# Kernel optimization log

Hardware: AMD Instinct MI355X
Metric: run time of the kernel (lower is better)

Reference implementation:

```python
import jax, jax.numpy as jnp
import numpy as np

B, S, D, K = 8, 2048, 512, 64

def setup_inputs() -> dict:
    key = jax.random.key(0)
    k1, k2, k3 = jax.random.split(key, 3)
    # glorot_uniform for weights, zeros for biases (matching Keras build)
    lim = float(np.sqrt(6.0 / (D + K)))
    return {
        "inputs": jax.random.normal(k1, (B, S, D), dtype=jnp.float32),
        "key_extract": jax.random.uniform(k2, (D, K), dtype=jnp.float32, minval=-lim, maxval=lim),
        "key_bias": jnp.zeros((1, K), dtype=jnp.float32),
        "query_extract": jax.random.uniform(k3, (D, K), dtype=jnp.float32, minval=-lim, maxval=lim),
        "query_bias": jnp.zeros((1, K), dtype=jnp.float32),
    }

def reference(inputs, key_extract, key_bias, query_extract, query_bias):
    # keys/query: [B, S, K]
    keys = jnp.einsum("bsd,dk->bsk", inputs, key_extract) + key_bias
    query = jnp.einsum("bsd,dk->bsk", inputs, query_extract) + query_bias
    # logits: [B, S, S] = query @ keys^T (no 1/sqrt(K) scaling in original)
    logits = jnp.einsum("bqk,bsk->bqs", query, keys)
    # NON-STANDARD: softmax over axis=1 (the query axis), not the last axis
    attn = jax.nn.softmax(logits, axis=1)
    # weighted_input: [B, S, D], raw inputs used as V
    return jnp.einsum("bqs,bsd->bqd", attn, inputs)
```

## Files before the change

### kernel.cpp

```cpp
#include <hip/hip_runtime.h>
#include <hip/hip_bf16.h>

#define Bn 8
#define Sn 2048
#define Dn 512
#define Kn 64

typedef _Float16 half8 __attribute__((ext_vector_type(8)));
typedef _Float16 half4v __attribute__((ext_vector_type(4)));
typedef __fp16 fp16x2 __attribute__((ext_vector_type(2)));
typedef float f32x4 __attribute__((ext_vector_type(4)));

#define MFMA16(a,b,c) __builtin_amdgcn_mfma_f32_16x16x32_f16(a,b,c,0,0,0)
#define LOG2E 1.4426950408889634f
#define EXP2(x) __builtin_amdgcn_exp2f(x)

__device__ __forceinline__ half8 ldfrag(const _Float16* base, int row, int k8){
    const int scol = k8 ^ (row & 7);
    return *(const half8*)((const char*)base + row*128 + scol*16);
}


__global__ __launch_bounds__(256) void wtrans_kernel(
    const float* __restrict__ Wk, const float* __restrict__ Wq,
    _Float16* __restrict__ Wt16)
{
    const int n = blockIdx.x;
    const int t = threadIdx.x;
    const float* src = (n < 64) ? Wq : Wk;
    const int nn = n & 63;
    #pragma unroll
    for (int i = 0; i < 2; ++i){
        const int k = t + 256*i;
        Wt16[(size_t)n*Dn + k] = (_Float16)src[(size_t)k*Kn + nn];
    }
}

__global__ __launch_bounds__(256, 2) void prep_kernel(
    const float* __restrict__ X, const _Float16* __restrict__ Wt16,
    const float* __restrict__ bk, const float* __restrict__ bq,
    _Float16* __restrict__ Qh2, _Float16* __restrict__ Kh2,
    _Float16* __restrict__ Vt2)
{
    __shared__ _Float16 Xt[2][32*64];
    const int bid = blockIdx.x;
    const int b = bid & 7, sb32 = bid >> 3;
    const int tid = threadIdx.x, lane = tid & 63, w = tid >> 6;
    const int l15 = lane & 15, l4 = lane >> 4;

    const int srow = tid >> 3, sg = tid & 7;
    const float* Xs = X + ((size_t)(b*Sn + sb32*32) + srow)*Dn + sg*8;
    const int sdst = srow*128 + (((sg ^ (srow & 7) ^ (srow >> 3)) & 7) * 16);

    const int n0 = w*32 + l15;
    const _Float16* Wp0 = Wt16 + (size_t)n0*Dn + l4*8;
    const _Float16* Wp1 = Wp0 + (size_t)16*Dn;

    f32x4 acc[2][2];
    #pragma unroll
    for (int i = 0; i < 2; ++i)
        #pragma unroll
        for (int j = 0; j < 2; ++j){ f32x4 z = {0.f,0.f,0.f,0.f}; acc[i][j] = z; }

    {
        const float4 v0 = *(const float4*)(Xs);
        const float4 v1 = *(const float4*)(Xs + 4);
        half8 h;
        h[0]=(_Float16)v0.x; h[1]=(_Float16)v0.y; h[2]=(_Float16)v0.z; h[3]=(_Float16)v0.w;
        h[4]=(_Float16)v1.x; h[5]=(_Float16)v1.y; h[6]=(_Float16)v1.z; h[7]=(_Float16)v1.w;
        *(half8*)((char*)Xt[0] + sdst) = h;
    }
    __syncthreads();

    const int dcol = w*16 + l15;
    #pragma unroll
    for (int kc = 0; kc < 8; ++kc){
        const _Float16* XtC = Xt[kc & 1];
        float4 nv0, nv1;
        if (kc < 7){
            nv0 = *(const float4*)(Xs + (kc+1)*64);
            nv1 = *(const float4*)(Xs + (kc+1)*64 + 4);
        }
        const half8 wf00 = *(const half8*)(Wp0 + kc*64);
        const half8 wf01 = *(const half8*)(Wp0 + kc*64 + 32);
        const half8 wf10 = *(const half8*)(Wp1 + kc*64);
        const half8 wf11 = *(const half8*)(Wp1 + kc*64 + 32);
        #pragma unroll
        for (int ks = 0; ks < 2; ++ks){
            #pragma unroll
            for (int qt = 0; qt < 2; ++qt){
                const int rw = qt*16 + l15;
                const int g = ((ks*4 + l4) ^ (rw & 7) ^ (rw >> 3)) & 7;
                const half8 a = *(const half8*)((const char*)XtC + rw*128 + g*16);
                acc[qt][0] = MFMA16(a, ks ? wf01 : wf00, acc[qt][0]);
                acc[qt][1] = MFMA16(a, ks ? wf11 : wf10, acc[qt][1]);
            }
        }
        {
            half8 hv;
            #pragma unroll
            for (int e = 0; e < 8; ++e){
                const int rw = l4*8 + e;
                const int g = ((dcol >> 3) ^ e ^ l4) & 7;
                hv[e] = XtC[rw*64 + g*8 + (dcol & 7)];
            }
            const size_t G = (((size_t)(b*32 + (sb32 >> 1))*2 + (sb32 & 1))*32 + kc*4 + w)*64 + lane;
            *(half8*)(Vt2 + G*8) = hv;
        }
        if (kc < 7){
            half8 h;
            h[0]=(_Float16)nv0.x; h[1]=(_Float16)nv0.y; h[2]=(_Float16)nv0.z; h[3]=(_Float16)nv0.w;
            h[4]=(_Float16)nv1.x; h[5]=(_Float16)nv1.y; h[6]=(_Float16)nv1.z; h[7]=(_Float16)nv1.w;
            *(half8*)((char*)Xt[(kc+1) & 1] + sdst) = h;
        }
        __syncthreads();
    }

    _Float16* tile16 = &Xt[0][0];
    #pragma unroll
    for (int qt = 0; qt < 2; ++qt){
        const int ql = qt*16 + l4*4;
        #pragma unroll
        for (int nt = 0; nt < 2; ++nt){
            const int n = w*32 + nt*16 + l15;
            const bool isQ = (n < 64);
            const float bias = isQ ? bq[n] : bk[n - 64];
            const float scale = isQ ? LOG2E : 1.0f;
            #pragma unroll
            for (int r = 0; r < 4; ++r)
                tile16[(ql + r)*128 + n] = (_Float16)((acc[qt][nt][r] + bias) * scale);
        }
    }
    __syncthreads();
    #pragma unroll
    for (int i = 0; i < 2; ++i){
        const int g = tid + 256*i;
        const int isK = g >> 8, qtl = (g >> 7) & 1, ks = (g >> 6) & 1, ln = g & 63;
        const int l4g = ln >> 4, l15g = ln & 15;
        const half8 h = *(const half8*)&tile16[(qtl*16 + l15g)*128 + isK*64 + ks*32 + l4g*8];
        const size_t tg = (size_t)b*128 + sb32*2 + qtl;
        _Float16* dst = (isK ? Kh2 : Qh2) + ((tg*2 + ks)*64 + ln)*8;
        *(half8*)dst = h;
    }
}

#define SBODY(QC0,QC1,QC2,QC3, QN0,QN1,QN2,QN3) do { \
    QN0 = *(const half8*)(Qp); \
    QN1 = *(const half8*)(Qp + 1024); \
    QN2 = *(const half8*)(Qp + 2048); \
    QN3 = *(const half8*)(Qp + 3072); \
    Qp += 8192; \
    f32x4 c0 = cinit, c1 = cinit; \
    c0 = MFMA16(ka0, QC0, c0); c0 = MFMA16(ka1, QC1, c0); \
    c1 = MFMA16(ka0, QC2, c1); c1 = MFMA16(ka1, QC3, c1); \
    _Pragma("unroll") \
    for (int r = 0; r < 4; ++r) \
        z[r] += EXP2(c0[r]) + EXP2(c1[r]); \
} while(0)

__global__ __launch_bounds__(512, 2) void stats_kernel(
    const _Float16* __restrict__ Qh2, const _Float16* __restrict__ Kh2,
    float* __restrict__ CS)
{
    __shared__ float zred[2][64];
    const int bid = blockIdx.x;
    const int b = bid & 7, stb = bid >> 3;
    const int tid = threadIdx.x, lane = tid & 63, w = tid >> 6;
    const int l15 = lane & 15, l4 = lane >> 4;
    const int sw = w & 3, qh = w >> 2, qh2 = qh*2;

    const half8 ka0 = *(const half8*)(Kh2 + ((size_t)((b*128 + stb*4 + sw)*2 + 0)*64 + lane)*8);
    const half8 ka1 = *(const half8*)(Kh2 + ((size_t)((b*128 + stb*4 + sw)*2 + 1)*64 + lane)*8);

    const char* Qp = (const char*)Qh2 + (size_t)(b*128 + qh2)*2048 + lane*16;

    const f32x4 cinit = {-64.f, -64.f, -64.f, -64.f};
    float z[4] = {0.f, 0.f, 0.f, 0.f};

    half8 qbA0, qbA1, qbA2, qbA3, qbB0, qbB1, qbB2, qbB3;
    qbA0 = *(const half8*)(Qp);
    qbA1 = *(const half8*)(Qp + 1024);
    qbA2 = *(const half8*)(Qp + 2048);
    qbA3 = *(const half8*)(Qp + 3072);
    Qp += 8192;

    for (int qc = 0; qc < 32; qc += 2){
        SBODY(qbA0,qbA1,qbA2,qbA3, qbB0,qbB1,qbB2,qbB3);
        SBODY(qbB0,qbB1,qbB2,qbB3, qbA0,qbA1,qbA2,qbA3);
    }
    #pragma unroll
    for (int d = 1; d < 16; d <<= 1)
        #pragma unroll
        for (int r = 0; r < 4; ++r)
            z[r] += __shfl_xor(z[r], d);
    if (l15 == 0){
        const int sl = sw*16 + l4*4;
        #pragma unroll
        for (int r = 0; r < 4; ++r) zred[qh][sl+r] = z[r];
    }
    __syncthreads();
    if (tid < 64)
        CS[b*Sn + stb*64 + tid] = -(64.0f + __log2f(zred[0][tid] + zred[1][tid]));
}

#define WRP(PT, QT, C) do { \
    const float e0 = EXP2(C[0]); \
    const float e1 = EXP2(C[1]); \
    const float e2 = EXP2(C[2]); \
    const float e3 = EXP2(C[3]); \
    const fp16x2 plo = __builtin_amdgcn_cvt_pkrtz(e0, e1); \
    const fp16x2 phi = __builtin_amdgcn_cvt_pkrtz(e2, e3); \
    uint2 pu; \
    pu.x = __builtin_bit_cast(unsigned int, plo); \
    pu.y = __builtin_bit_cast(unsigned int, phi); \
    *(uint2*)((char*)(PT) + (QT)*2048 + pw_base) = pu; \
} while(0)

#define ABODY(KA, KAN, VB, VBN, CSA, CSN, PT) do { \
    f32x4 c0 = {CSA.x, CSA.y, CSA.z, CSA.w}; \
    f32x4 c1 = c0, c2 = c0, c3 = c0; \
    c0 = MFMA16(KA[0], qb[0][0], c0); c0 = MFMA16(KA[1], qb[0][1], c0); \
    c1 = MFMA16(KA[0], qb[1][0], c1); c1 = MFMA16(KA[1], qb[1][1], c1); \
    c2 = MFMA16(KA[0], qb[2][0], c2); c2 = MFMA16(KA[1], qb[2][1], c2); \
    c3 = MFMA16(KA[0], qb[3][0], c3); c3 = MFMA16(KA[1], qb[3][1], c3); \
    KAN[0] = *(const half8*)(Kp); \
    KAN[1] = *(const half8*)(Kp + 1024); \
    Kp += 8192; \
    CSN = *(const float4*)Cp; Cp += 64; \
    WRP(PT, 0, c0); WRP(PT, 1, c1); \
    WRP(PT, 2, c2); WRP(PT, 3, c3); \
    asm volatile("s_waitcnt lgkmcnt(0)\n\ts_barrier" ::: "memory"); \
    _Pragma("unroll") \
    for (int d_ = 0; d_ < 4; ++d_){ \
        VBN[d_]   = *(const half8*)(Vp0 + d_*1024); \
        VBN[4+d_] = *(const half8*)(Vp1 + d_*1024); \
    } \
    Vp0 += 65536; Vp1 += 65536; \
    __builtin_amdgcn_s_setprio(1); \
    { const char* PB = (const char*)(PT); \
      _Pragma("unroll") \
      for (int ks = 0; ks < 2; ++ks){ \
        const int po = ks ? paoff1 : paoff0; \
        const half8 pa0 = *(const half8*)(PB + 0*2048 + po); \
        const half8 pa1 = *(const half8*)(PB + 1*2048 + po); \
        const half8 pa2 = *(const half8*)(PB + 2*2048 + po); \
        const half8 pa3 = *(const half8*)(PB + 3*2048 + po); \
        _Pragma("unroll") \
        for (int d_ = 0; d_ < 4; ++d_){ \
            acc[0][d_] = MFMA16(pa0, VB[ks*4+d_], acc[0][d_]); \
            acc[1][d_] = MFMA16(pa1, VB[ks*4+d_], acc[1][d_]); \
            acc[2][d_] = MFMA16(pa2, VB[ks*4+d_], acc[2][d_]); \
            acc[3][d_] = MFMA16(pa3, VB[ks*4+d_], acc[3][d_]); \
        } \
      } } \
    __builtin_amdgcn_s_setprio(0); \
} while(0)

__global__ __launch_bounds__(256, 2) void attn_kernel(
    const _Float16* __restrict__ Qh2, const _Float16* __restrict__ Kh2,
    const _Float16* __restrict__ Vt2, const float* __restrict__ CS,
    float* __restrict__ out)
{
    __shared__ _Float16 Pt[2][64*64];
    const int bid = blockIdx.x;
    const int b  = bid & 7;
    const int qi = (bid >> 3) & 31;
    const int dh = bid >> 8;
    const int q0 = qi * 64;
    const int tid = threadIdx.x, lane = tid & 63, w = tid >> 6;
    const int l15 = lane & 15, l4 = lane >> 4;
    const int soff = w*16 + l4*4;
    const int sb2  = soff * 2;
    const int pw_base = l15*128 + (sb2 ^ ((l15 & 7) << 4));
    const int paoff0  = l15*128 + ((l4 ^ (l15 & 7)) << 4);
    const int paoff1  = paoff0 ^ 64;

    const size_t qgb = (size_t)b*128 + qi*4;
    half8 qb[4][2];
    #pragma unroll
    for (int qt = 0; qt < 4; ++qt)
        #pragma unroll
        for (int ks = 0; ks < 2; ++ks)
            qb[qt][ks] = *(const half8*)(Qh2 + (((qgb + qt)*2 + ks)*64 + lane)*8);

    const char* Kp  = (const char*)Kh2 + (size_t)(b*128 + w)*2048 + lane*16;
    const char* Vp0 = (const char*)Vt2 + (size_t)(b*2048 + dh*16 + w*4)*1024 + lane*16;
    const char* Vp1 = Vp0 + 32768;
    const float* Cp = CS + b*Sn + soff;

    half8 kaA[2], kaB[2], vbA[8], vbB[8];
    float4 csA, csB;
    kaA[0] = *(const half8*)(Kp);
    kaA[1] = *(const half8*)(Kp + 1024);
    Kp += 8192;
    #pragma unroll
    for (int d_ = 0; d_ < 4; ++d_){
        vbA[d_]   = *(const half8*)(Vp0 + d_*1024);
        vbA[4+d_] = *(const half8*)(Vp1 + d_*1024);
    }
    Vp0 += 65536; Vp1 += 65536;
    csA = *(const float4*)Cp; Cp += 64;

    f32x4 acc[4][4];
    #pragma unroll
    for (int i = 0; i < 4; ++i)
        #pragma unroll
        for (int j = 0; j < 4; ++j){ f32x4 zz4 = {0.f,0.f,0.f,0.f}; acc[i][j] = zz4; }

    for (int it = 0; it < 16; ++it){
        ABODY(kaA, kaB, vbA, vbB, csA, csB, Pt[0]);
        ABODY(kaB, kaA, vbB, vbA, csB, csA, Pt[1]);
    }

    float* ob = out + (size_t)(b*Sn + q0)*Dn + dh*256 + w*64;
    #pragma unroll
    for (int qt = 0; qt < 4; ++qt){
        const int q = qt*16 + l4*4;
        #pragma unroll
        for (int d_ = 0; d_ < 4; ++d_){
            #pragma unroll
            for (int r = 0; r < 4; ++r)
                ob[(size_t)(q + r)*Dn + d_*16 + l15] = acc[qt][d_][r];
        }
    }
}

extern "C" void kernel_launch(void* const* d_in, const int* in_sizes, int n_in,
                              void* d_out, int out_size, void* d_ws, size_t ws_size,
                              hipStream_t stream)
{
    const float* X  = (const float*)d_in[0];
    const float* Wk = (const float*)d_in[1];
    const float* bk = (const float*)d_in[2];
    const float* Wq = (const float*)d_in[3];
    const float* bq = (const float*)d_in[4];
    float* out = (float*)d_out;

    char* ws = (char*)d_ws;
    _Float16* Qh2  = (_Float16*)ws;
    _Float16* Kh2  = (_Float16*)(ws + ((size_t)2 << 20));
    _Float16* Vt2  = (_Float16*)(ws + ((size_t)4 << 20));
    float*    CS   = (float*)(ws + ((size_t)20 << 20));
    _Float16* Wt16 = (_Float16*)(ws + ((size_t)20 << 20) + (2 << 16));

    wtrans_kernel<<<dim3(128), dim3(256), 0, stream>>>(Wk, Wq, Wt16);
    prep_kernel<<<dim3(Bn*(Sn/32)), dim3(256), 0, stream>>>(X, Wt16, bk, bq, Qh2, Kh2, Vt2);
    stats_kernel<<<dim3(Bn*(Sn/64)), dim3(512), 0, stream>>>(Qh2, Kh2, CS);
    attn_kernel<<<dim3(Bn*(Sn/64)*2), dim3(256), 0, stream>>>(Qh2, Kh2, Vt2, CS, out);
}
```

Measured before the change: 73.73 us.

## Process two 64-key tiles per barrier step in attention kernel

Doubles the key-tile width handled per loop step from 64 to 128 keys. P is written to a larger 64x128 shared tile with a new swizzle, so only one barrier is needed per 128 keys instead of per 64. The V loads are split into a mid-step load and a next-step prefetch. This halves the barrier count and gives more MFMA work between syncs, at the cost of more registers (extra K fragments and V buffers) and twice the LDS, which may reduce occupancy below 2 blocks per CU.

```diff
diff --git a/kernel.cpp b/kernel.cpp
--- a/kernel.cpp
+++ b/kernel.cpp
@@ -203,7 +203,7 @@
         CS[b*Sn + stb*64 + tid] = -(64.0f + __log2f(zred[0][tid] + zred[1][tid]));
 }
 
-#define WRP(PT, QT, C) do { \
+#define WRP(PT, QT, C, PWO) do { \
     const float e0 = EXP2(C[0]); \
     const float e1 = EXP2(C[1]); \
     const float e2 = EXP2(C[2]); \
@@ -213,44 +213,83 @@
     uint2 pu; \
     pu.x = __builtin_bit_cast(unsigned int, plo); \
     pu.y = __builtin_bit_cast(unsigned int, phi); \
-    *(uint2*)((char*)(PT) + (QT)*2048 + pw_base) = pu; \
+    *(uint2*)((char*)(PT) + (QT)*4096 + (PWO)) = pu; \
 } while(0)
 
-#define ABODY(KA, KAN, VB, VBN, CSA, CSN, PT) do { \
-    f32x4 c0 = {CSA.x, CSA.y, CSA.z, CSA.w}; \
+#define SSTEP(PT, KA, KAN, CSA0, CSA1, CSN0, CSN1, VC, VN) do { \
+    __builtin_amdgcn_s_setprio(1); \
+    f32x4 c0 = {CSA0.x, CSA0.y, CSA0.z, CSA0.w}; \
     f32x4 c1 = c0, c2 = c0, c3 = c0; \
     c0 = MFMA16(KA[0], qb[0][0], c0); c0 = MFMA16(KA[1], qb[0][1], c0); \
     c1 = MFMA16(KA[0], qb[1][0], c1); c1 = MFMA16(KA[1], qb[1][1], c1); \
     c2 = MFMA16(KA[0], qb[2][0], c2); c2 = MFMA16(KA[1], qb[2][1], c2); \
     c3 = MFMA16(KA[0], qb[3][0], c3); c3 = MFMA16(KA[1], qb[3][1], c3); \
+    f32x4 d0 = {CSA1.x, CSA1.y, CSA1.z, CSA1.w}; \
+    f32x4 d1 = d0, d2 = d0, d3 = d0; \
+    d0 = MFMA16(KA[2], qb[0][0], d0); d0 = MFMA16(KA[3], qb[0][1], d0); \
+    d1 = MFMA16(KA[2], qb[1][0], d1); d1 = MFMA16(KA[3], qb[1][1], d1); \
+    d2 = MFMA16(KA[2], qb[2][0], d2); d2 = MFMA16(KA[3], qb[2][1], d2); \
+    d3 = MFMA16(KA[2], qb[3][0], d3); d3 = MFMA16(KA[3], qb[3][1], d3); \
+    __builtin_amdgcn_s_setprio(0); \
     KAN[0] = *(const half8*)(Kp); \
     KAN[1] = *(const half8*)(Kp + 1024); \
-    Kp += 8192; \
-    CSN = *(const float4*)Cp; Cp += 64; \
-    WRP(PT, 0, c0); WRP(PT, 1, c1); \
-    WRP(PT, 2, c2); WRP(PT, 3, c3); \
+    KAN[2] = *(const half8*)(Kp + 8192); \
+    KAN[3] = *(const half8*)(Kp + 8192 + 1024); \
+    Kp += 16384; \
+    CSN0 = *(const float4*)Cp; \
+    CSN1 = *(const float4*)(Cp + 64); \
+    Cp += 128; \
+    WRP(PT, 0, c0, pw0); WRP(PT, 1, c1, pw0); \
+    WRP(PT, 2, c2, pw0); WRP(PT, 3, c3, pw0); \
+    WRP(PT, 0, d0, pw1); WRP(PT, 1, d1, pw1); \
+    WRP(PT, 2, d2, pw1); WRP(PT, 3, d3, pw1); \
     asm volatile("s_waitcnt lgkmcnt(0)\n\ts_barrier" ::: "memory"); \
+    half8 vm[8]; \
     _Pragma("unroll") \
     for (int d_ = 0; d_ < 4; ++d_){ \
-        VBN[d_]   = *(const half8*)(Vp0 + d_*1024); \
-        VBN[4+d_] = *(const half8*)(Vp1 + d_*1024); \
+        vm[d_]   = *(const half8*)(Vp0 + d_*1024); \
+        vm[4+d_] = *(const half8*)(Vp1 + d_*1024); \
     } \
     Vp0 += 65536; Vp1 += 65536; \
     __builtin_amdgcn_s_setprio(1); \
     { const char* PB = (const char*)(PT); \
       _Pragma("unroll") \
       for (int ks = 0; ks < 2; ++ks){ \
-        const int po = ks ? paoff1 : paoff0; \
-        const half8 pa0 = *(const half8*)(PB + 0*2048 + po); \
-        const half8 pa1 = *(const half8*)(PB + 1*2048 + po); \
-        const half8 pa2 = *(const half8*)(PB + 2*2048 + po); \
-        const half8 pa3 = *(const half8*)(PB + 3*2048 + po); \
+        const int po = pa[ks]; \
+        const half8 pa0 = *(const half8*)(PB + 0*4096 + po); \
+        const half8 pa1 = *(const half8*)(PB + 1*4096 + po); \
+        const half8 pa2 = *(const half8*)(PB + 2*4096 + po); \
+        const half8 pa3 = *(const half8*)(PB + 3*4096 + po); \
         _Pragma("unroll") \
         for (int d_ = 0; d_ < 4; ++d_){ \
-            acc[0][d_] = MFMA16(pa0, VB[ks*4+d_], acc[0][d_]); \
-            acc[1][d_] = MFMA16(pa1, VB[ks*4+d_], acc[1][d_]); \
-            acc[2][d_] = MFMA16(pa2, VB[ks*4+d_], acc[2][d_]); \
-            acc[3][d_] = MFMA16(pa3, VB[ks*4+d_], acc[3][d_]); \
+            acc[0][d_] = MFMA16(pa0, VC[ks*4+d_], acc[0][d_]); \
+            acc[1][d_] = MFMA16(pa1, VC[ks*4+d_], acc[1][d_]); \
+            acc[2][d_] = MFMA16(pa2, VC[ks*4+d_], acc[2][d_]); \
+            acc[3][d_] = MFMA16(pa3, VC[ks*4+d_], acc[3][d_]); \
+        } \
+      } } \
+    __builtin_amdgcn_s_setprio(0); \
+    _Pragma("unroll") \
+    for (int d_ = 0; d_ < 4; ++d_){ \
+        VN[d_]   = *(const half8*)(Vp0 + d_*1024); \
+        VN[4+d_] = *(const half8*)(Vp1 + d_*1024); \
+    } \
+    Vp0 += 65536; Vp1 += 65536; \
+    __builtin_amdgcn_s_setprio(1); \
+    { const char* PB = (const char*)(PT); \
+      _Pragma("unroll") \
+      for (int ks = 0; ks < 2; ++ks){ \
+        const int po = pa[2+ks]; \
+        const half8 pa0 = *(const half8*)(PB + 0*4096 + po); \
+        const half8 pa1 = *(const half8*)(PB + 1*4096 + po); \
+        const half8 pa2 = *(const half8*)(PB + 2*4096 + po); \
+        const half8 pa3 = *(const half8*)(PB + 3*4096 + po); \
+        _Pragma("unroll") \
+        for (int d_ = 0; d_ < 4; ++d_){ \
+            acc[0][d_] = MFMA16(pa0, vm[ks*4+d_], acc[0][d_]); \
+            acc[1][d_] = MFMA16(pa1, vm[ks*4+d_], acc[1][d_]); \
+            acc[2][d_] = MFMA16(pa2, vm[ks*4+d_], acc[2][d_]); \
+            acc[3][d_] = MFMA16(pa3, vm[ks*4+d_], acc[3][d_]); \
         } \
       } } \
     __builtin_amdgcn_s_setprio(0); \
@@ -261,7 +300,7 @@
     const _Float16* __restrict__ Vt2, const float* __restrict__ CS,
     float* __restrict__ out)
 {
-    __shared__ _Float16 Pt[2][64*64];
+    __shared__ _Float16 Pt[2][64*128];
     const int bid = blockIdx.x;
     const int b  = bid & 7;
     const int qi = (bid >> 3) & 31;
@@ -270,10 +309,13 @@
     const int tid = threadIdx.x, lane = tid & 63, w = tid >> 6;
     const int l15 = lane & 15, l4 = lane >> 4;
     const int soff = w*16 + l4*4;
-    const int sb2  = soff * 2;
-    const int pw_base = l15*128 + (sb2 ^ ((l15 & 7) << 4));
-    const int paoff0  = l15*128 + ((l4 ^ (l15 & 7)) << 4);
-    const int paoff1  = paoff0 ^ 64;
+
+    const int pw0 = l15*256 + (((w*2 + (l4 >> 1)) ^ (l15 & 7)) << 4) + ((l4 & 1) << 3);
+    const int pw1 = pw0 + 128;
+    int pa[4];
+    #pragma unroll
+    for (int j = 0; j < 4; ++j)
+        pa[j] = l15*256 + (((j >> 1)*8 + (((j & 1)*4 + l4) ^ (l15 & 7))) << 4);
 
     const size_t qgb = (size_t)b*128 + qi*4;
     half8 qb[4][2];
@@ -288,18 +330,22 @@
     const char* Vp1 = Vp0 + 32768;
     const float* Cp = CS + b*Sn + soff;
 
-    half8 kaA[2], kaB[2], vbA[8], vbB[8];
-    float4 csA, csB;
+    half8 kaA[4], kaB[4], vbA[8], vbB[8];
+    float4 csA0, csA1, csB0, csB1;
     kaA[0] = *(const half8*)(Kp);
     kaA[1] = *(const half8*)(Kp + 1024);
-    Kp += 8192;
+    kaA[2] = *(const half8*)(Kp + 8192);
+    kaA[3] = *(const half8*)(Kp + 8192 + 1024);
+    Kp += 16384;
+    csA0 = *(const float4*)Cp;
+    csA1 = *(const float4*)(Cp + 64);
+    Cp += 128;
     #pragma unroll
     for (int d_ = 0; d_ < 4; ++d_){
         vbA[d_]   = *(const half8*)(Vp0 + d_*1024);
         vbA[4+d_] = *(const half8*)(Vp1 + d_*1024);
     }
     Vp0 += 65536; Vp1 += 65536;
-    csA = *(const float4*)Cp; Cp += 64;
 
     f32x4 acc[4][4];
     #pragma unroll
@@ -307,9 +353,9 @@
         #pragma unroll
         for (int j = 0; j < 4; ++j){ f32x4 zz4 = {0.f,0.f,0.f,0.f}; acc[i][j] = zz4; }
 
-    for (int it = 0; it < 16; ++it){
-        ABODY(kaA, kaB, vbA, vbB, csA, csB, Pt[0]);
-        ABODY(kaB, kaA, vbB, vbA, csB, csA, Pt[1]);
+    for (int it = 0; it < 8; ++it){
+        SSTEP(Pt[0], kaA, kaB, csA0, csA1, csB0, csB1, vbA, vbB);
+        SSTEP(Pt[1], kaB, kaA, csB0, csB1, csA0, csA1, vbB, vbA);
     }
 
     float* ob = out + (size_t)(b*Sn + q0)*Dn + dh*256 + w*64;
```

Measured after the change: 74.70 us. No clear change (+1.3%).

## Split stats kernel over query chunks with LDS-staged Q and partial-sum finalize

Applied to the files above, without the earlier changes.

The column-softmax stats pass now has each block load a 256-query chunk of Q into LDS with direct global-to-LDS loads. Each wave keeps four key tiles in registers and reuses every Q fragment across them, instead of streaming the full Q from global memory per key tile. Partial exp sums per query chunk go to a workspace buffer, and a new small kernel adds them and takes the log. This cuts redundant Q traffic and raises register reuse per MFMA, at the cost of an extra kernel launch, more register pressure and a workspace round trip.

```diff
diff --git a/kernel.cpp b/kernel.cpp
--- a/kernel.cpp
+++ b/kernel.cpp
@@ -14,6 +14,12 @@
 #define MFMA16(a,b,c) __builtin_amdgcn_mfma_f32_16x16x32_f16(a,b,c,0,0,0)
 #define LOG2E 1.4426950408889634f
 #define EXP2(x) __builtin_amdgcn_exp2f(x)
+
+__device__ __forceinline__ void glds16(const void* g, void* l){
+    __builtin_amdgcn_global_load_lds(
+        (const __attribute__((address_space(1))) unsigned int*)g,
+        (__attribute__((address_space(3))) unsigned int*)l, 16, 0, 0);
+}
 
 __device__ __forceinline__ half8 ldfrag(const _Float16* base, int row, int k8){
     const int scol = k8 ^ (row & 7);
@@ -144,63 +150,78 @@
     }
 }
 
-#define SBODY(QC0,QC1,QC2,QC3, QN0,QN1,QN2,QN3) do { \
-    QN0 = *(const half8*)(Qp); \
-    QN1 = *(const half8*)(Qp + 1024); \
-    QN2 = *(const half8*)(Qp + 2048); \
-    QN3 = *(const half8*)(Qp + 3072); \
-    Qp += 8192; \
-    f32x4 c0 = cinit, c1 = cinit; \
-    c0 = MFMA16(ka0, QC0, c0); c0 = MFMA16(ka1, QC1, c0); \
-    c1 = MFMA16(ka0, QC2, c1); c1 = MFMA16(ka1, QC3, c1); \
-    _Pragma("unroll") \
-    for (int r = 0; r < 4; ++r) \
-        z[r] += EXP2(c0[r]) + EXP2(c1[r]); \
-} while(0)
-
-__global__ __launch_bounds__(512, 2) void stats_kernel(
+__global__ __launch_bounds__(512) void stats_kernel(
     const _Float16* __restrict__ Qh2, const _Float16* __restrict__ Kh2,
-    float* __restrict__ CS)
-{
-    __shared__ float zred[2][64];
+    float* __restrict__ Zp)
+{
+    __shared__ _Float16 Qs[256*64];
     const int bid = blockIdx.x;
-    const int b = bid & 7, stb = bid >> 3;
+    const int b = bid & 7, ss = (bid >> 3) & 3, qc = bid >> 5;
     const int tid = threadIdx.x, lane = tid & 63, w = tid >> 6;
     const int l15 = lane & 15, l4 = lane >> 4;
-    const int sw = w & 3, qh = w >> 2, qh2 = qh*2;
-
-    const half8 ka0 = *(const half8*)(Kh2 + ((size_t)((b*128 + stb*4 + sw)*2 + 0)*64 + lane)*8);
-    const half8 ka1 = *(const half8*)(Kh2 + ((size_t)((b*128 + stb*4 + sw)*2 + 1)*64 + lane)*8);
-
-    const char* Qp = (const char*)Qh2 + (size_t)(b*128 + qh2)*2048 + lane*16;
+
+    const char* Qsrc = (const char*)Qh2 + (size_t)(b*128 + qc*16)*2048;
+    #pragma unroll
+    for (int i = 0; i < 4; ++i)
+        glds16(Qsrc + tid*16 + i*8192, (char*)Qs + w*1024 + i*8192);
+
+    half8 ka[4][2];
+    const char* Kb = (const char*)Kh2 + (size_t)(b*128 + ss*32 + w*4)*2048 + lane*16;
+    #pragma unroll
+    for (int st = 0; st < 4; ++st)
+        #pragma unroll
+        for (int ks = 0; ks < 2; ++ks)
+            ka[st][ks] = *(const half8*)(Kb + st*2048 + ks*1024);
+
+    __syncthreads();
 
     const f32x4 cinit = {-64.f, -64.f, -64.f, -64.f};
-    float z[4] = {0.f, 0.f, 0.f, 0.f};
-
-    half8 qbA0, qbA1, qbA2, qbA3, qbB0, qbB1, qbB2, qbB3;
-    qbA0 = *(const half8*)(Qp);
-    qbA1 = *(const half8*)(Qp + 1024);
-    qbA2 = *(const half8*)(Qp + 2048);
-    qbA3 = *(const half8*)(Qp + 3072);
-    Qp += 8192;
-
-    for (int qc = 0; qc < 32; qc += 2){
-        SBODY(qbA0,qbA1,qbA2,qbA3, qbB0,qbB1,qbB2,qbB3);
-        SBODY(qbB0,qbB1,qbB2,qbB3, qbA0,qbA1,qbA2,qbA3);
+    float z[4][4];
+    #pragma unroll
+    for (int st = 0; st < 4; ++st)
+        #pragma unroll
+        for (int r = 0; r < 4; ++r) z[st][r] = 0.f;
+
+    const char* Qb = (const char*)Qs + lane*16;
+    for (int qt = 0; qt < 16; ++qt){
+        const half8 qb0 = *(const half8*)(Qb + qt*2048);
+        const half8 qb1 = *(const half8*)(Qb + qt*2048 + 1024);
+        #pragma unroll
+        for (int st = 0; st < 4; ++st){
+            f32x4 c = cinit;
+            c = MFMA16(ka[st][0], qb0, c);
+            c = MFMA16(ka[st][1], qb1, c);
+            #pragma unroll
+            for (int r = 0; r < 4; ++r)
+                z[st][r] += EXP2(c[r]);
+        }
     }
     #pragma unroll
     for (int d = 1; d < 16; d <<= 1)
         #pragma unroll
-        for (int r = 0; r < 4; ++r)
-            z[r] += __shfl_xor(z[r], d);
+        for (int st = 0; st < 4; ++st)
+            #pragma unroll
+            for (int r = 0; r < 4; ++r)
+                z[st][r] += __shfl_xor(z[st][r], d);
     if (l15 == 0){
-        const int sl = sw*16 + l4*4;
-        #pragma unroll
-        for (int r = 0; r < 4; ++r) zred[qh][sl+r] = z[r];
-    }
-    __syncthreads();
-    if (tid < 64)
-        CS[b*Sn + stb*64 + tid] = -(64.0f + __log2f(zred[0][tid] + zred[1][tid]));
+        float* zp = Zp + (((size_t)(qc*8 + b)) << 11) + ss*512 + w*64 + l4*4;
+        #pragma unroll
+        for (int st = 0; st < 4; ++st)
+            #pragma unroll
+            for (int r = 0; r < 4; ++r)
+                zp[st*16 + r] = z[st][r];
+    }
+}
+
+__global__ __launch_bounds__(256) void csfin_kernel(
+    const float* __restrict__ Zp, float* __restrict__ CS)
+{
+    const int idx = blockIdx.x*256 + threadIdx.x;
+    float zsum = 0.f;
+    #pragma unroll
+    for (int qc = 0; qc < 8; ++qc)
+        zsum += Zp[(qc << 14) + idx];
+    CS[idx] = -(64.0f + __log2f(zsum));
 }
 
 #define WRP(PT, QT, C) do { \
@@ -342,9 +363,11 @@
     _Float16* Vt2  = (_Float16*)(ws + ((size_t)4 << 20));
     float*    CS   = (float*)(ws + ((size_t)20 << 20));
     _Float16* Wt16 = (_Float16*)(ws + ((size_t)20 << 20) + (2 << 16));
+    float*    Zp   = (float*)(ws + ((size_t)21 << 20));
 
     wtrans_kernel<<<dim3(128), dim3(256), 0, stream>>>(Wk, Wq, Wt16);
     prep_kernel<<<dim3(Bn*(Sn/32)), dim3(256), 0, stream>>>(X, Wt16, bk, bq, Qh2, Kh2, Vt2);
-    stats_kernel<<<dim3(Bn*(Sn/64)), dim3(512), 0, stream>>>(Qh2, Kh2, CS);
+    stats_kernel<<<dim3(256), dim3(512), 0, stream>>>(Qh2, Kh2, Zp);
+    csfin_kernel<<<dim3(64), dim3(256), 0, stream>>>(Zp, CS);
     attn_kernel<<<dim3(Bn*(Sn/64)*2), dim3(256), 0, stream>>>(Qh2, Kh2, Vt2, CS, out);
 }
```

Result: faster. 68.95 us (-6.5%).
